# Optimization experiments

Hardware: AMD Instinct MI355X
Metric: run time of the kernel (lower is better)

Reference implementation:

```python
import jax, jax.numpy as jnp
import numpy as np

B = 2
D = H = W = 28
WS = 7          # window size
SHIFT = 3       # shift size
DIM = 192
HEADS = 6
HEAD_DIM = DIM // HEADS
SCALE = HEAD_DIM ** -0.5
N = WS ** 3                      # 343 tokens per window
NW = (D // WS) ** 3              # 64 windows per batch element
MLP_HID = int(DIM * 4.0)
EPS = 1e-5


def _rel_index():
    coords = np.stack(np.meshgrid(np.arange(WS), np.arange(WS), np.arange(WS), indexing='ij'))
    cf = coords.reshape(3, -1)                       # (3, N)
    rel = (cf[:, :, None] - cf[:, None, :]).transpose(1, 2, 0)  # (N, N, 3)
    rel[..., 0] += WS - 1
    rel[..., 1] += WS - 1
    rel[..., 2] += WS - 1
    rel[..., 0] *= (2 * WS - 1) ** 2
    rel[..., 1] *= (2 * WS - 1)
    return rel.sum(-1).astype(np.int32)             # (N, N)


def _attn_mask():
    # standard 3D Swin shift mask: 0 within region, -100 across regions
    img = np.zeros((1, D, H, W, 1), dtype=np.float32)
    cnt = 0
    sl = (slice(0, -WS), slice(-WS, -SHIFT), slice(-SHIFT, None))
    for d in sl:
        for h in sl:
            for w in sl:
                img[:, d, h, w, :] = cnt
                cnt += 1
    mw = img.reshape(1, D // WS, WS, H // WS, WS, W // WS, WS, 1)
    mw = mw.transpose(0, 1, 3, 5, 2, 4, 6, 7).reshape(-1, N)      # (NW, N)
    diff = mw[:, None, :] - mw[:, :, None]
    return np.where(diff != 0, np.float32(-100.0), np.float32(0.0))


def _win_part(x):
    b = x.shape[0]
    x = x.reshape(b, D // WS, WS, H // WS, WS, W // WS, WS, DIM)
    return x.transpose(0, 1, 3, 5, 2, 4, 6, 7).reshape(-1, N, DIM)


def _win_rev(wins):
    x = wins.reshape(B, D // WS, H // WS, W // WS, WS, WS, WS, DIM)
    return x.transpose(0, 1, 4, 2, 5, 3, 6, 7).reshape(B, D, H, W, DIM)


def _ln(x, g, b):
    m = jnp.mean(x, axis=-1, keepdims=True)
    v = jnp.mean((x - m) ** 2, axis=-1, keepdims=True)
    return (x - m) * jax.lax.rsqrt(v + EPS) * g + b


def setup_inputs() -> dict:
    key = jax.random.key(0)
    ks = jax.random.split(key, 8)
    std = 0.02
    table_len = (2 * WS - 1) ** 3
    return {
        'x': jax.random.normal(ks[0], (B, D * H * W, DIM), jnp.float32),
        'mask_matrix': jnp.asarray(_attn_mask()),
        'rel_index': jnp.asarray(_rel_index()),
        'rel_bias_table': jax.random.normal(ks[1], (table_len, HEADS), jnp.float32) * std,
        'norm1_g': jnp.ones((DIM,), jnp.float32),
        'norm1_b': jnp.zeros((DIM,), jnp.float32),
        'qkv_w': jax.random.normal(ks[2], (3 * DIM, DIM), jnp.float32) * std,
        'qkv_b': jnp.zeros((3 * DIM,), jnp.float32),
        'proj_w': jax.random.normal(ks[3], (DIM, DIM), jnp.float32) * std,
        'proj_b': jnp.zeros((DIM,), jnp.float32),
        'norm2_g': jnp.ones((DIM,), jnp.float32),
        'norm2_b': jnp.zeros((DIM,), jnp.float32),
        'fc1_w': jax.random.normal(ks[4], (MLP_HID, DIM), jnp.float32) * std,
        'fc1_b': jnp.zeros((MLP_HID,), jnp.float32),
        'fc2_w': jax.random.normal(ks[5], (DIM, MLP_HID), jnp.float32) * std,
        'fc2_b': jnp.zeros((DIM,), jnp.float32),
    }


def reference(x, mask_matrix, rel_index, rel_bias_table, norm1_g, norm1_b,
              qkv_w, qkv_b, proj_w, proj_b, norm2_g, norm2_b,
              fc1_w, fc1_b, fc2_w, fc2_b):
    shortcut = x
    h = _ln(x, norm1_g, norm1_b).reshape(B, D, H, W, DIM)
    h = jnp.roll(h, (-SHIFT, -SHIFT, -SHIFT), axis=(1, 2, 3))
    wins = _win_part(h)                                  # (B*NW, N, C)
    qkv = wins @ qkv_w.T + qkv_b                         # (B*NW, N, 3C)
    qkv = qkv.reshape(-1, N, 3, HEADS, HEAD_DIM).transpose(2, 0, 3, 1, 4)
    q, k, v = qkv[0] * SCALE, qkv[1], qkv[2]             # (B*NW, H, N, d)
    attn = jnp.einsum('bhnd,bhmd->bhnm', q, k)
    bias = rel_bias_table[rel_index.reshape(-1)].reshape(N, N, HEADS).transpose(2, 0, 1)
    attn = attn + bias[None]
    attn = attn.reshape(B, NW, HEADS, N, N) + mask_matrix[None, :, None]
    attn = jax.nn.softmax(attn.reshape(-1, HEADS, N, N), axis=-1)
    out = jnp.einsum('bhnm,bhmd->bhnd', attn, v)
    out = out.transpose(0, 2, 1, 3).reshape(-1, N, DIM)
    out = out @ proj_w.T + proj_b
    h = _win_rev(out)                                    # (B, D, H, W, C)
    h = jnp.roll(h, (SHIFT, SHIFT, SHIFT), axis=(1, 2, 3)).reshape(B, D * H * W, DIM)
    x = shortcut + h
    y = _ln(x, norm2_g, norm2_b)
    y = jax.nn.gelu(y @ fc1_w.T + fc1_b, approximate=False) @ fc2_w.T + fc2_b
    return x + y
```

## Files before the change

### kernel.cpp

```cpp
#include <hip/hip_runtime.h>
#include <hip/hip_bf16.h>
#include <math.h>

#define DIMC 192
#define NTOK 343
#define NHEADS 6
#define HD 32
#define NN 117649
#define MLP 768
#define MTOT 43904
#define QSCALE 0.17677669529663687f

#define WS_WGT    1453056
#define OFF_QKVW  0
#define OFF_PROJW 110592
#define OFF_FC1W  147456
#define OFF_FC2W  294912
#define NWGT      442368
#define WS_CHUNK  2337792

typedef __attribute__((ext_vector_type(8))) short bf16x8;
typedef __attribute__((ext_vector_type(4))) float f32x4;

__device__ __forceinline__ float b2f(__hip_bfloat16 v) { return __bfloat162float(v); }
__device__ __forceinline__ __hip_bfloat16 f2b(float v) { return __float2bfloat16(v); }
__device__ __forceinline__ unsigned short bfu(float v) {
    __hip_bfloat16 b = f2b(v);
    return *(unsigned short*)&b;
}

__device__ __forceinline__ float2 bfp2(unsigned u) {
    union { unsigned i; float f; } a, b;
    a.i = u << 16;
    b.i = u & 0xffff0000u;
    return make_float2(a.f, b.f);
}

__device__ __forceinline__ int win_to_tok(int w, int n) {
    int bb = w >> 6, widx = w & 63;
    int wd = widx >> 4, wh = (widx >> 2) & 3, ww = widx & 3;
    int sd = n / 49, r = n - sd * 49;
    int sh = r / 7, sw = r - sh * 7;
    int gd = wd * 7 + sd + 3; if (gd >= 28) gd -= 28;
    int gh = wh * 7 + sh + 3; if (gh >= 28) gh -= 28;
    int gw = ww * 7 + sw + 3; if (gw >= 28) gw -= 28;
    return bb * 21952 + gd * 784 + gh * 28 + gw;
}

__device__ __forceinline__ int region_of(int widx, int n) {
    int wd = widx >> 4, wh = (widx >> 2) & 3, ww = widx & 3;
    int sd = n / 49, rr = n - sd * 49;
    int sh = rr / 7, sw = rr - sh * 7;
    int cd = wd * 7 + sd, ch = wh * 7 + sh, cw = ww * 7 + sw;
    int dsl = (cd < 21) ? 0 : ((cd < 25) ? 1 : 2);
    int hsl = (ch < 21) ? 0 : ((ch < 25) ? 1 : 2);
    int wsl = (cw < 21) ? 0 : ((cw < 25) ? 1 : 2);
    return dsl * 9 + hsl * 3 + wsl;
}

__global__ __launch_bounds__(256) void bias_kernel(
    const int* __restrict__ rel, const float* __restrict__ table,
    __hip_bfloat16* __restrict__ biasQ) {
    int idx = blockIdx.x * 256 + threadIdx.x;
    if (idx >= NN) return;
    int m = idx / NTOK, q = idx - m * NTOK;
    int ri = rel[q * NTOK + m];
    #pragma unroll
    for (int h = 0; h < NHEADS; h++)
        biasQ[(((size_t)h * 88 + (m >> 2)) * 344 + q) * 4 + (m & 3)] = f2b(table[ri * NHEADS + h]);
}

__global__ __launch_bounds__(256) void wconv_kernel(
    const float* __restrict__ qkv_w, const float* __restrict__ proj_w,
    const float* __restrict__ fc1_w, const float* __restrict__ fc2_w,
    __hip_bfloat16* __restrict__ Wb) {
    int i = blockIdx.x * 256 + threadIdx.x;
    if (i >= NWGT) return;
    float v;
    if      (i < OFF_PROJW) v = qkv_w[i - OFF_QKVW];
    else if (i < OFF_FC1W)  v = proj_w[i - OFF_PROJW];
    else if (i < OFF_FC2W)  v = fc1_w[i - OFF_FC1W];
    else                    v = fc2_w[i - OFF_FC2W];
    Wb[i] = f2b(v);
}

__global__ __launch_bounds__(256) void ln1_kernel(
    const float* __restrict__ x, const float* __restrict__ g,
    const float* __restrict__ bt, __hip_bfloat16* __restrict__ wins,
    int w0, int Mrows) {
    int t = blockIdx.x * 4 + (threadIdx.x >> 6);
    if (t >= Mrows) return;
    int lane = threadIdx.x & 63;
    int wl = t / NTOK, n = t - wl * NTOK;
    int tok = win_to_tok(w0 + wl, n);
    const float* xp = x + (size_t)tok * DIMC;
    float v0 = xp[lane], v1 = xp[lane + 64], v2 = xp[lane + 128];
    float s = v0 + v1 + v2, s2 = v0 * v0 + v1 * v1 + v2 * v2;
    #pragma unroll
    for (int m = 32; m >= 1; m >>= 1) { s += __shfl_xor(s, m, 64); s2 += __shfl_xor(s2, m, 64); }
    float mean = s * (1.f / 192.f);
    float var = s2 * (1.f / 192.f) - mean * mean;
    float r = rsqrtf(var + 1e-5f);
    __hip_bfloat16* op = wins + (size_t)t * DIMC;
    op[lane]       = f2b((v0 - mean) * r * g[lane]       + bt[lane]);
    op[lane + 64]  = f2b((v1 - mean) * r * g[lane + 64]  + bt[lane + 64]);
    op[lane + 128] = f2b((v2 - mean) * r * g[lane + 128] + bt[lane + 128]);
}

__global__ __launch_bounds__(256) void ln2_kernel(
    const float* __restrict__ x2, const float* __restrict__ g,
    const float* __restrict__ bt, __hip_bfloat16* __restrict__ y, int r0g) {
    int t = blockIdx.x * 4 + (threadIdx.x >> 6);
    int lane = threadIdx.x & 63;
    const float* xp = x2 + (size_t)(r0g + t) * DIMC;
    float v0 = xp[lane], v1 = xp[lane + 64], v2 = xp[lane + 128];
    float s = v0 + v1 + v2, s2 = v0 * v0 + v1 * v1 + v2 * v2;
    #pragma unroll
    for (int m = 32; m >= 1; m >>= 1) { s += __shfl_xor(s, m, 64); s2 += __shfl_xor(s2, m, 64); }
    float mean = s * (1.f / 192.f);
    float var = s2 * (1.f / 192.f) - mean * mean;
    float r = rsqrtf(var + 1e-5f);
    __hip_bfloat16* op = y + (size_t)t * DIMC;
    op[lane]       = f2b((v0 - mean) * r * g[lane]       + bt[lane]);
    op[lane + 64]  = f2b((v1 - mean) * r * g[lane + 64]  + bt[lane + 64]);
    op[lane + 128] = f2b((v2 - mean) * r * g[lane + 128] + bt[lane + 128]);
}

template <int EPI>
__global__ __launch_bounds__(256) void gemm_kernel(
    const __hip_bfloat16* __restrict__ A, const __hip_bfloat16* __restrict__ Bw,
    const float* __restrict__ bias, int K, int Mrows, int w0, int r0g,
    const float* __restrict__ shortcut, float* __restrict__ xout,
    void* __restrict__ out_p) {
    __shared__ __align__(16) __hip_bfloat16 As[256 * 32];
    __shared__ __align__(16) __hip_bfloat16 Bs[64 * 32];
    int tid = threadIdx.x;
    int wave = tid >> 6, lane = tid & 63;
    int quad = lane >> 4, r = lane & 15;
    int row0 = blockIdx.y * 256, col0 = blockIdx.x * 64;
    int lrow = lane >> 2, lcol = (lane & 3) * 8;
    f32x4 acc[4][4];
    #pragma unroll
    for (int mi = 0; mi < 4; mi++)
        #pragma unroll
        for (int ni = 0; ni < 4; ni++) acc[mi][ni] = (f32x4){0.f, 0.f, 0.f, 0.f};
    for (int k0 = 0; k0 < K; k0 += 32) {
        #pragma unroll
        for (int inst = 0; inst < 4; inst++) {
            int rowl = wave * 64 + inst * 16 + lrow;
            int ar = row0 + rowl; if (ar >= Mrows) ar = Mrows - 1;
            *(uint4*)&As[rowl * 32 + lcol] = *(const uint4*)(A + (size_t)ar * K + k0 + lcol);
        }
        {
            int rowb = wave * 16 + lrow;
            *(uint4*)&Bs[rowb * 32 + lcol] = *(const uint4*)(Bw + (size_t)(col0 + rowb) * K + k0 + lcol);
        }
        __syncthreads();
        bf16x8 af[4], bf[4];
        #pragma unroll
        for (int mi = 0; mi < 4; mi++)
            af[mi] = *(const bf16x8*)&As[(wave * 64 + mi * 16 + r) * 32 + quad * 8];
        #pragma unroll
        for (int ni = 0; ni < 4; ni++)
            bf[ni] = *(const bf16x8*)&Bs[(ni * 16 + r) * 32 + quad * 8];
        #pragma unroll
        for (int mi = 0; mi < 4; mi++)
            #pragma unroll
            for (int ni = 0; ni < 4; ni++)
                acc[mi][ni] = __builtin_amdgcn_mfma_f32_16x16x32_bf16(af[mi], bf[ni], acc[mi][ni], 0, 0, 0);
        __syncthreads();
    }
    #pragma unroll
    for (int mi = 0; mi < 4; mi++) {
        #pragma unroll
        for (int i = 0; i < 4; i++) {
            int rloc = wave * 64 + mi * 16 + quad * 4 + i;
            int rr = row0 + rloc;
            if (rr >= Mrows) continue;
            #pragma unroll
            for (int ni = 0; ni < 4; ni++) {
                int c = col0 + ni * 16 + r;
                float v = acc[mi][ni][i] + bias[c];
                if (EPI == 0) {
                    int wl = rr / NTOK, n = rr - wl * NTOK;
                    int t = c / DIMC, rem = c - t * DIMC;
                    int hh = rem >> 5, d = rem & 31;
                    if (t == 0) v *= QSCALE;
                    ((__hip_bfloat16*)out_p)[((((size_t)wl * NHEADS + hh) * 3 + t) * NTOK + n) * HD + d] = f2b(v);
                } else if (EPI == 1) {
                    int wl = rr / NTOK, n = rr - wl * NTOK;
                    size_t tok = (size_t)win_to_tok(w0 + wl, n);
                    xout[tok * DIMC + c] = v + shortcut[tok * DIMC + c];
                } else if (EPI == 2) {
                    float gel = 0.5f * v * (1.0f + erff(v * 0.70710678118654752f));
                    ((__hip_bfloat16*)out_p)[(size_t)rr * MLP + c] = f2b(gel);
                } else {
                    size_t gi = (size_t)(r0g + rr) * DIMC + c;
                    xout[gi] += v;
                }
            }
        }
    }
}

__global__ __launch_bounds__(256) void attn_kernel(
    const __hip_bfloat16* __restrict__ qkv, const __hip_bfloat16* __restrict__ biasQ,
    __hip_bfloat16* __restrict__ out, int w0) {
    int wl = blockIdx.x / NHEADS, h = blockIdx.x - wl * NHEADS;
    int wm = (w0 + wl) & 63;
    __shared__ __align__(16) unsigned VtU[32 * 180];
    __shared__ unsigned char regS[NTOK];
    const __hip_bfloat16* base = qkv + ((size_t)(wl * NHEADS + h) * 3) * NTOK * HD;
    const __hip_bfloat16* Kp = base + NTOK * HD;
    const unsigned* Vp = (const unsigned*)(base + 2 * NTOK * HD);
    int tid = threadIdx.x;
    for (int i = tid; i < NTOK; i += 256) regS[i] = (unsigned char)region_of(wm, i);
    for (int u = tid; u < 176 * 16; u += 256) {
        int m2 = u >> 4, dp = u & 15;
        unsigned a = 0, b = 0;
        if (m2 <= 170)      { a = Vp[(2 * m2) * 16 + dp]; b = Vp[(2 * m2 + 1) * 16 + dp]; }
        else if (m2 == 171) { a = Vp[342 * 16 + dp]; }
        VtU[(2 * dp) * 180 + m2]     = (a & 0xffffu) | (b << 16);
        VtU[(2 * dp + 1) * 180 + m2] = (a >> 16) | (b & 0xffff0000u);
    }
    __syncthreads();
    int wave = tid >> 6, lane = tid & 63;
    int quad = lane >> 4, r = lane & 15;
    const __hip_bfloat16* vt = (const __hip_bfloat16*)&VtU[0];
    for (int qt = wave; qt < 22; qt += 4) {
        int q0 = qt * 16;
        int qc = q0 + r; if (qc > 342) qc = 342;
        bf16x8 qf = *(const bf16x8*)(base + (size_t)qc * HD + quad * 8);
        int rq = regS[qc];
        float S[22][4];
        #pragma unroll
        for (int mt = 0; mt < 22; mt++) {
            int mr = mt * 16 + r; if (mr > 342) mr = 342;
            bf16x8 kf = *(const bf16x8*)(Kp + (size_t)mr * HD + quad * 8);
            f32x4 c = {0.f, 0.f, 0.f, 0.f};
            c = __builtin_amdgcn_mfma_f32_16x16x32_bf16(kf, qf, c, 0, 0, 0);
            uint2 bu = *(const uint2*)(biasQ + (((size_t)h * 88 + mt * 4 + quad) * 344 + qc) * 4);
            float2 blo = bfp2(bu.x), bhi = bfp2(bu.y);
            float bv[4] = {blo.x, blo.y, bhi.x, bhi.y};
            #pragma unroll
            for (int i = 0; i < 4; i++) {
                int m = mt * 16 + quad * 4 + i;
                if (m < NTOK) {
                    float msk = (regS[m] == rq) ? 0.f : -100.f;
                    S[mt][i] = c[i] + bv[i] + msk;
                } else S[mt][i] = -1e30f;
            }
        }
        float mx = -1e30f;
        #pragma unroll
        for (int mt = 0; mt < 22; mt++)
            #pragma unroll
            for (int i = 0; i < 4; i++) mx = fmaxf(mx, S[mt][i]);
        mx = fmaxf(mx, __shfl_xor(mx, 16, 64));
        mx = fmaxf(mx, __shfl_xor(mx, 32, 64));
        float l = 0.f;
        #pragma unroll
        for (int mt = 0; mt < 22; mt++)
            #pragma unroll
            for (int i = 0; i < 4; i++) { float p = __expf(S[mt][i] - mx); S[mt][i] = p; l += p; }
        l += __shfl_xor(l, 16, 64);
        l += __shfl_xor(l, 32, 64);
        float rl = 1.f / l;
        int Pn[22][2];
        #pragma unroll
        for (int mt = 0; mt < 22; mt++) {
            Pn[mt][0] = (int)((unsigned)bfu(S[mt][0] * rl) | ((unsigned)bfu(S[mt][1] * rl) << 16));
            Pn[mt][1] = (int)((unsigned)bfu(S[mt][2] * rl) | ((unsigned)bfu(S[mt][3] * rl) << 16));
        }
        f32x4 o0 = {0.f, 0.f, 0.f, 0.f}, o1 = {0.f, 0.f, 0.f, 0.f};
        bool hiQuad = (quad >= 2);
        int srcBase = (quad & 1) * 32 + r;
        #pragma unroll
        for (int ch = 0; ch < 11; ch++) {
            unsigned afu[4];
            #pragma unroll
            for (int k = 0; k < 4; k++) {
                int src = srcBase + (k >> 1) * 16;
                int lo = __shfl(Pn[2 * ch][k & 1], src, 64);
                int hi = __shfl(Pn[2 * ch + 1][k & 1], src, 64);
                afu[k] = (unsigned)(hiQuad ? hi : lo);
            }
            bf16x8 pf = *(bf16x8*)afu;
            bf16x8 v0 = *(const bf16x8*)(vt + (size_t)r * 360 + ch * 32 + quad * 8);
            bf16x8 v1 = *(const bf16x8*)(vt + (size_t)(r + 16) * 360 + ch * 32 + quad * 8);
            o0 = __builtin_amdgcn_mfma_f32_16x16x32_bf16(pf, v0, o0, 0, 0, 0);
            o1 = __builtin_amdgcn_mfma_f32_16x16x32_bf16(pf, v1, o1, 0, 0, 0);
        }
        #pragma unroll
        for (int i = 0; i < 4; i++) {
            int q = q0 + quad * 4 + i;
            if (q < NTOK) {
                __hip_bfloat16* orow = out + ((size_t)wl * NTOK + q) * DIMC + h * HD;
                orow[r] = f2b(o0[i]);
                orow[r + 16] = f2b(o1[i]);
            }
        }
    }
}

extern "C" void kernel_launch(void* const* d_in, const int* in_sizes, int n_in,
                              void* d_out, int out_size, void* d_ws, size_t ws_size,
                              hipStream_t stream) {
    const float* x      = (const float*)d_in[0];
    const int*   relidx = (const int*)d_in[2];
    const float* table  = (const float*)d_in[3];
    const float* n1g    = (const float*)d_in[4];
    const float* n1b    = (const float*)d_in[5];
    const float* qkv_w  = (const float*)d_in[6];
    const float* qkv_b  = (const float*)d_in[7];
    const float* proj_w = (const float*)d_in[8];
    const float* proj_b = (const float*)d_in[9];
    const float* n2g    = (const float*)d_in[10];
    const float* n2b    = (const float*)d_in[11];
    const float* fc1_w  = (const float*)d_in[12];
    const float* fc1_b  = (const float*)d_in[13];
    const float* fc2_w  = (const float*)d_in[14];
    const float* fc2_b  = (const float*)d_in[15];

    char* ws = (char*)d_ws;
    __hip_bfloat16* biasQ = (__hip_bfloat16*)ws;
    __hip_bfloat16* Wb    = (__hip_bfloat16*)(ws + WS_WGT);
    float* out = (float*)d_out;

    int W = 1;
    {
        const int cand[7] = {64, 32, 16, 8, 4, 2, 1};
        for (int i = 0; i < 7; i++)
            if ((size_t)WS_CHUNK + (size_t)cand[i] * 526848 <= ws_size) { W = cand[i]; break; }
    }
    int R = 64;
    {
        const int cand[9] = {43904, 21952, 10976, 6272, 3136, 896, 448, 128, 64};
        for (int i = 0; i < 9; i++)
            if ((size_t)WS_CHUNK + (size_t)cand[i] * 1920 <= ws_size) { R = cand[i]; break; }
    }
    __hip_bfloat16* R0  = (__hip_bfloat16*)(ws + WS_CHUNK);
    __hip_bfloat16* QKV = (__hip_bfloat16*)(ws + WS_CHUNK + (size_t)W * 131712);
    __hip_bfloat16* Y   = (__hip_bfloat16*)(ws + WS_CHUNK);
    __hip_bfloat16* HID = (__hip_bfloat16*)(ws + WS_CHUNK + (size_t)R * 384);

    bias_kernel<<<(NN + 255) / 256, 256, 0, stream>>>(relidx, table, biasQ);
    wconv_kernel<<<(NWGT + 255) / 256, 256, 0, stream>>>(qkv_w, proj_w, fc1_w, fc2_w, Wb);

    int mch = W * NTOK;
    int gy = (mch + 255) / 256;
    int gln = (mch + 3) / 4;
    for (int c = 0; c < 128 / W; c++) {
        int w0 = c * W;
        ln1_kernel<<<gln, 256, 0, stream>>>(x, n1g, n1b, R0, w0, mch);
        gemm_kernel<0><<<dim3(9, gy), 256, 0, stream>>>(
            R0, Wb + OFF_QKVW, qkv_b, DIMC, mch, w0, 0, nullptr, nullptr, QKV);
        attn_kernel<<<W * NHEADS, 256, 0, stream>>>(QKV, biasQ, R0, w0);
        gemm_kernel<1><<<dim3(3, gy), 256, 0, stream>>>(
            R0, Wb + OFF_PROJW, proj_b, DIMC, mch, w0, 0, x, out, nullptr);
    }
    for (int m = 0; m < MTOT / R; m++) {
        int r0g = m * R;
        int gyr = (R + 255) / 256;
        ln2_kernel<<<R / 4, 256, 0, stream>>>(out, n2g, n2b, Y, r0g);
        gemm_kernel<2><<<dim3(12, gyr), 256, 0, stream>>>(
            Y, Wb + OFF_FC1W, fc1_b, DIMC, R, 0, 0, nullptr, nullptr, HID);
        gemm_kernel<3><<<dim3(3, gyr), 256, 0, stream>>>(
            HID, Wb + OFF_FC2W, fc2_b, MLP, R, 0, r0g, nullptr, out, nullptr);
    }
}
```

Measured before the change: 488.4 us.

## Stage K in LDS, drop softmax max pass, split query tiles, async GEMM loads

The GEMM tile loads now use global_load_lds to copy global memory straight into shared memory, bypassing registers. The attention kernel stages K in LDS with zero padding and computes exp without subtracting the row max, which removes the S register array and the max reduction. Normalization is deferred to the output by shuffling 1/l per row. The attention grid gets a second dimension that splits the 22 query tiles into two halves, adding blocks at the cost of a duplicated K/V staging load, and the window chunk size may grow to 128. Skipping the max subtraction risks overflow if the logits are large, and the direct-to-LDS loads rely on a per-lane layout that must match the old indexing.

After: 521.8 us. +6.8%, slower.

```diff
diff --git a/kernel.cpp b/kernel.cpp
--- a/kernel.cpp
+++ b/kernel.cpp
@@ -21,6 +21,12 @@
 
 typedef __attribute__((ext_vector_type(8))) short bf16x8;
 typedef __attribute__((ext_vector_type(4))) float f32x4;
+
+typedef const unsigned __attribute__((address_space(1)))* gas1_t;
+typedef unsigned __attribute__((address_space(3)))* las3_t;
+__device__ __forceinline__ void gld16(const void* g, void* l) {
+    __builtin_amdgcn_global_load_lds((gas1_t)g, (las3_t)l, 16, 0, 0);
+}
 
 __device__ __forceinline__ float b2f(__hip_bfloat16 v) { return __bfloat162float(v); }
 __device__ __forceinline__ __hip_bfloat16 f2b(float v) { return __float2bfloat16(v); }
@@ -149,11 +155,11 @@
         for (int inst = 0; inst < 4; inst++) {
             int rowl = wave * 64 + inst * 16 + lrow;
             int ar = row0 + rowl; if (ar >= Mrows) ar = Mrows - 1;
-            *(uint4*)&As[rowl * 32 + lcol] = *(const uint4*)(A + (size_t)ar * K + k0 + lcol);
+            gld16(A + (size_t)ar * K + k0 + lcol, &As[(wave * 64 + inst * 16) * 32]);
         }
         {
             int rowb = wave * 16 + lrow;
-            *(uint4*)&Bs[rowb * 32 + lcol] = *(const uint4*)(Bw + (size_t)(col0 + rowb) * K + k0 + lcol);
+            gld16(Bw + (size_t)(col0 + rowb) * K + k0 + lcol, &Bs[(wave * 16) * 32]);
         }
         __syncthreads();
         bf16x8 af[4], bf[4];
@@ -208,13 +214,19 @@
     __hip_bfloat16* __restrict__ out, int w0) {
     int wl = blockIdx.x / NHEADS, h = blockIdx.x - wl * NHEADS;
     int wm = (w0 + wl) & 63;
+    int y = blockIdx.y;
+    __shared__ __align__(16) __hip_bfloat16 Ks[352 * 32];
     __shared__ __align__(16) unsigned VtU[32 * 180];
-    __shared__ unsigned char regS[NTOK];
+    __shared__ unsigned char regS[352];
     const __hip_bfloat16* base = qkv + ((size_t)(wl * NHEADS + h) * 3) * NTOK * HD;
     const __hip_bfloat16* Kp = base + NTOK * HD;
     const unsigned* Vp = (const unsigned*)(base + 2 * NTOK * HD);
     int tid = threadIdx.x;
-    for (int i = tid; i < NTOK; i += 256) regS[i] = (unsigned char)region_of(wm, i);
+    for (int i = tid; i < 352; i += 256) regS[i] = (i < NTOK) ? (unsigned char)region_of(wm, i) : 255;
+    for (int u = tid; u < 1408; u += 256) {
+        uint4 v = (u < 1372) ? ((const uint4*)Kp)[u] : make_uint4(0, 0, 0, 0);
+        ((uint4*)Ks)[u] = v;
+    }
     for (int u = tid; u < 176 * 16; u += 256) {
         int m2 = u >> 4, dp = u & 15;
         unsigned a = 0, b = 0;
@@ -227,51 +239,35 @@
     int wave = tid >> 6, lane = tid & 63;
     int quad = lane >> 4, r = lane & 15;
     const __hip_bfloat16* vt = (const __hip_bfloat16*)&VtU[0];
-    for (int qt = wave; qt < 22; qt += 4) {
+    for (int qt = y * 11 + wave; qt < (y + 1) * 11; qt += 4) {
         int q0 = qt * 16;
         int qc = q0 + r; if (qc > 342) qc = 342;
         bf16x8 qf = *(const bf16x8*)(base + (size_t)qc * HD + quad * 8);
         int rq = regS[qc];
-        float S[22][4];
+        float l = 0.f;
+        int Pn[22][2];
         #pragma unroll
         for (int mt = 0; mt < 22; mt++) {
-            int mr = mt * 16 + r; if (mr > 342) mr = 342;
-            bf16x8 kf = *(const bf16x8*)(Kp + (size_t)mr * HD + quad * 8);
+            bf16x8 kf = *(const bf16x8*)(Ks + (mt * 16 + r) * 32 + quad * 8);
             f32x4 c = {0.f, 0.f, 0.f, 0.f};
             c = __builtin_amdgcn_mfma_f32_16x16x32_bf16(kf, qf, c, 0, 0, 0);
             uint2 bu = *(const uint2*)(biasQ + (((size_t)h * 88 + mt * 4 + quad) * 344 + qc) * 4);
             float2 blo = bfp2(bu.x), bhi = bfp2(bu.y);
             float bv[4] = {blo.x, blo.y, bhi.x, bhi.y};
+            float p[4];
             #pragma unroll
             for (int i = 0; i < 4; i++) {
                 int m = mt * 16 + quad * 4 + i;
-                if (m < NTOK) {
-                    float msk = (regS[m] == rq) ? 0.f : -100.f;
-                    S[mt][i] = c[i] + bv[i] + msk;
-                } else S[mt][i] = -1e30f;
+                float msk = (regS[m] == rq) ? 0.f : -100.f;
+                p[i] = __expf(c[i] + bv[i] + msk);
+                l += p[i];
             }
-        }
-        float mx = -1e30f;
-        #pragma unroll
-        for (int mt = 0; mt < 22; mt++)
-            #pragma unroll
-            for (int i = 0; i < 4; i++) mx = fmaxf(mx, S[mt][i]);
-        mx = fmaxf(mx, __shfl_xor(mx, 16, 64));
-        mx = fmaxf(mx, __shfl_xor(mx, 32, 64));
-        float l = 0.f;
-        #pragma unroll
-        for (int mt = 0; mt < 22; mt++)
-            #pragma unroll
-            for (int i = 0; i < 4; i++) { float p = __expf(S[mt][i] - mx); S[mt][i] = p; l += p; }
+            Pn[mt][0] = (int)((unsigned)bfu(p[0]) | ((unsigned)bfu(p[1]) << 16));
+            Pn[mt][1] = (int)((unsigned)bfu(p[2]) | ((unsigned)bfu(p[3]) << 16));
+        }
         l += __shfl_xor(l, 16, 64);
         l += __shfl_xor(l, 32, 64);
         float rl = 1.f / l;
-        int Pn[22][2];
-        #pragma unroll
-        for (int mt = 0; mt < 22; mt++) {
-            Pn[mt][0] = (int)((unsigned)bfu(S[mt][0] * rl) | ((unsigned)bfu(S[mt][1] * rl) << 16));
-            Pn[mt][1] = (int)((unsigned)bfu(S[mt][2] * rl) | ((unsigned)bfu(S[mt][3] * rl) << 16));
-        }
         f32x4 o0 = {0.f, 0.f, 0.f, 0.f}, o1 = {0.f, 0.f, 0.f, 0.f};
         bool hiQuad = (quad >= 2);
         int srcBase = (quad & 1) * 32 + r;
@@ -291,13 +287,16 @@
             o0 = __builtin_amdgcn_mfma_f32_16x16x32_bf16(pf, v0, o0, 0, 0, 0);
             o1 = __builtin_amdgcn_mfma_f32_16x16x32_bf16(pf, v1, o1, 0, 0, 0);
         }
+        float rli[4];
+        #pragma unroll
+        for (int i = 0; i < 4; i++) rli[i] = __shfl(rl, quad * 4 + i, 64);
         #pragma unroll
         for (int i = 0; i < 4; i++) {
             int q = q0 + quad * 4 + i;
             if (q < NTOK) {
                 __hip_bfloat16* orow = out + ((size_t)wl * NTOK + q) * DIMC + h * HD;
-                orow[r] = f2b(o0[i]);
-                orow[r + 16] = f2b(o1[i]);
+                orow[r] = f2b(o0[i] * rli[i]);
+                orow[r + 16] = f2b(o1[i] * rli[i]);
             }
         }
     }
@@ -329,8 +328,8 @@
 
     int W = 1;
     {
-        const int cand[7] = {64, 32, 16, 8, 4, 2, 1};
-        for (int i = 0; i < 7; i++)
+        const int cand[8] = {128, 64, 32, 16, 8, 4, 2, 1};
+        for (int i = 0; i < 8; i++)
             if ((size_t)WS_CHUNK + (size_t)cand[i] * 526848 <= ws_size) { W = cand[i]; break; }
     }
     int R = 64;
@@ -355,7 +354,7 @@
         ln1_kernel<<<gln, 256, 0, stream>>>(x, n1g, n1b, R0, w0, mch);
         gemm_kernel<0><<<dim3(9, gy), 256, 0, stream>>>(
             R0, Wb + OFF_QKVW, qkv_b, DIMC, mch, w0, 0, nullptr, nullptr, QKV);
-        attn_kernel<<<W * NHEADS, 256, 0, stream>>>(QKV, biasQ, R0, w0);
+        attn_kernel<<<dim3(W * NHEADS, 2), 256, 0, stream>>>(QKV, biasQ, R0, w0);
         gemm_kernel<1><<<dim3(3, gy), 256, 0, stream>>>(
             R0, Wb + OFF_PROJW, proj_b, DIMC, mch, w0, 0, x, out, nullptr);
     }
```
